# Kernel optimization log

Hardware: AMD Instinct MI355X
Metric: run time of the kernel (lower is better)

The kernel has to match this reference:

```python
import jax, jax.numpy as jnp
import numpy as np

N_HEAD = 8
N_FEAT = 256
CHUNK = 64          # window/chunk size N
D_K = N_FEAT // N_HEAD
SCALE = D_K ** (-0.5)
B_ = 2048           # batch * nChunkNum
NCHUNK = 128        # nChunkNum (B_ % NCHUNK == 0)


def setup_inputs() -> dict:
    key = jax.random.key(0)
    ks = jax.random.split(key, 12)
    f32 = jnp.float32
    query = jax.random.normal(ks[0], (B_, CHUNK, N_FEAT), f32)
    key_t = jax.random.normal(ks[1], (B_, CHUNK, N_FEAT), f32)
    value = jax.random.normal(ks[2], (B_, CHUNK, N_FEAT), f32)
    # padding mask (B_, time2): multiplicative 0/1 floats
    mask = jax.random.randint(ks[3], (B_, CHUNK), 0, 2).astype(f32)
    # shifted-chunk additive mask (nChunkNum, N, N): 0 for neighbors, -100 otherwise
    cm_bin = jax.random.randint(ks[4], (NCHUNK, CHUNK, CHUNK), 0, 2)
    chunk_mask = jnp.where(cm_bin == 1, 0.0, -100.0).astype(f32)
    def lin(k):
        return jax.random.normal(k, (N_FEAT, N_FEAT), f32) * 0.02
    Wq, Wk, Wv, Wo = lin(ks[5]), lin(ks[6]), lin(ks[7]), lin(ks[8])
    bq = jnp.zeros((N_FEAT,), f32)
    bk = jnp.zeros((N_FEAT,), f32)
    bv = jnp.zeros((N_FEAT,), f32)
    bo = jnp.zeros((N_FEAT,), f32)
    rpb_table = jax.random.normal(ks[9], (2 * CHUNK - 1, N_HEAD), f32) * 0.02
    return {"query": query, "key": key_t, "value": value, "mask": mask,
            "chunk_mask": chunk_mask, "Wq": Wq, "bq": bq, "Wk": Wk, "bk": bk,
            "Wv": Wv, "bv": bv, "Wo": Wo, "bo": bo, "rpb_table": rpb_table}


def _rel_pos_index():
    # index[i, j] = (i - j) + CHUNK - 1, shape (N, N)
    w = jnp.arange(CHUNK)
    return w[:, None] - w[None, :] + (CHUNK - 1)


def reference(query, key, value, mask, chunk_mask, Wq, bq, Wk, bk, Wv, bv, Wo, bo, rpb_table):
    B, N, _ = query.shape
    # qkv projections -> (B, h, N, d_k)
    def proj(x, W, b):
        y = x @ W.T + b
        return y.reshape(B, N, N_HEAD, D_K).transpose(0, 2, 1, 3)
    q = proj(query, Wq, bq)
    k = proj(key, Wk, bk)
    v = proj(value, Wv, bv)
    # windowed attention scores (B, h, N, N)
    scores = jnp.einsum("bhid,bhjd->bhij", q, k) * SCALE
    # relative position bias: gather (N, N, h) -> (h, N, N)
    rpb = rpb_table[_rel_pos_index()].transpose(2, 0, 1)
    scores = scores + rpb[None]
    # padding mask: multiply, then fill zeros with -100 (as in torch source)
    scores = scores * mask[:, None, None, :]
    scores = jnp.where(scores == 0, jnp.float32(-100.0), scores)
    # additive shifted-chunk mask
    nC = chunk_mask.shape[0]
    scores = scores.reshape(B // nC, nC, N_HEAD, N, N) + chunk_mask[None, :, None]
    scores = scores.reshape(B, N_HEAD, N, N)
    attn = jax.nn.softmax(scores, axis=-1)
    x = jnp.einsum("bhij,bhjd->bhid", attn, v)          # (B, h, N, d_k)
    x = x.transpose(0, 2, 1, 3).reshape(B, N, N_FEAT)     # (B, N, n_feat)
    return x @ Wo.T + bo
```

## Files before the change

### kernel.cpp

```cpp
#include <hip/hip_runtime.h>
#include <hip/hip_bf16.h>

typedef __bf16 bf16_t;
typedef __bf16 bf16x8 __attribute__((ext_vector_type(8)));
typedef __bf16 bf16x4 __attribute__((ext_vector_type(4)));
typedef float f32x4 __attribute__((ext_vector_type(4)));

#define OFF_A   0
#define OFF_B   32768
#define OFF_RPB 65536
#define OFF_CMM (65536 + 4096)
#define OFF_PAD (65536 + 4096 + 512)
#define SMEM_BYTES (65536 + 4096 + 512 + 8)

__device__ __forceinline__ int tile_off(int r, int c) {
  return (r << 9) + ((((c >> 3) ^ (r & 7)) << 4) | ((c & 7) << 1));
}
__device__ __forceinline__ int vt_off(int d, int j) {
  return (d << 7) + ((((j >> 3) ^ (d & 7)) << 4) | ((j & 7) << 1));
}
__device__ __forceinline__ int ps_off(int i, int j) {
  return (i << 6) + ((((j >> 3) ^ ((i >> 1) & 3)) << 4) | ((j & 7) << 1));
}

template <int UNROLL>
__device__ __forceinline__ void stage_x(const float* __restrict__ src, char* __restrict__ dst, int tid) {
  const float4* s4 = (const float4*)src;
#pragma unroll
  for (int kk = 0; kk < 8; kk += UNROLL) {
    float4 v[UNROLL];
#pragma unroll
    for (int u = 0; u < UNROLL; ++u) v[u] = s4[tid + ((kk + u) << 9)];
#pragma unroll
    for (int u = 0; u < UNROLL; ++u) {
      int f = tid + ((kk + u) << 9);
      int row = f >> 6;
      int col = (f & 63) << 2;
      bf16x4 p;
      p[0] = (bf16_t)v[u].x; p[1] = (bf16_t)v[u].y; p[2] = (bf16_t)v[u].z; p[3] = (bf16_t)v[u].w;
      *(bf16x4*)(dst + tile_off(row, col)) = p;
    }
  }
}

__device__ __forceinline__ void gemm_tile(const char* __restrict__ sA, const bf16_t* __restrict__ W,
                                          int cb, int l15, int g, f32x4 acc[4][2]) {
#pragma unroll
  for (int kt = 0; kt < 8; ++kt) {
    bf16x8 a[4];
#pragma unroll
    for (int mt = 0; mt < 4; ++mt)
      a[mt] = *(const bf16x8*)(sA + tile_off(mt*16 + l15, kt*32 + g*8));
#pragma unroll
    for (int nt = 0; nt < 2; ++nt) {
      bf16x8 bw = *(const bf16x8*)(W + (cb + nt*16 + l15)*256 + kt*32 + g*8);
#pragma unroll
      for (int mt = 0; mt < 4; ++mt)
        acc[mt][nt] = __builtin_amdgcn_mfma_f32_16x16x32_bf16(a[mt], bw, acc[mt][nt], 0, 0, 0);
    }
  }
}

__device__ __forceinline__ void gemm_tile2(const char* __restrict__ sA, const char* __restrict__ sB,
                                           const bf16_t* __restrict__ W0, const bf16_t* __restrict__ W1,
                                           int cb, int l15, int g,
                                           f32x4 acc0[4][2], f32x4 acc1[4][2]) {
  const bf16_t* w0p = W0 + (cb + l15)*256 + g*8;
  const bf16_t* w1p = W1 + (cb + l15)*256 + g*8;
#pragma unroll
  for (int kt = 0; kt < 8; ++kt) {
    bf16x8 a0[4], a1[4];
#pragma unroll
    for (int mt = 0; mt < 4; ++mt) {
      a0[mt] = *(const bf16x8*)(sA + tile_off(mt*16 + l15, kt*32 + g*8));
      a1[mt] = *(const bf16x8*)(sB + tile_off(mt*16 + l15, kt*32 + g*8));
    }
#pragma unroll
    for (int nt = 0; nt < 2; ++nt) {
      bf16x8 bw0 = *(const bf16x8*)(w0p + nt*16*256 + kt*32);
      bf16x8 bw1 = *(const bf16x8*)(w1p + nt*16*256 + kt*32);
#pragma unroll
      for (int mt = 0; mt < 4; ++mt) {
        acc0[mt][nt] = __builtin_amdgcn_mfma_f32_16x16x32_bf16(a0[mt], bw0, acc0[mt][nt], 0, 0, 0);
        acc1[mt][nt] = __builtin_amdgcn_mfma_f32_16x16x32_bf16(a1[mt], bw1, acc1[mt][nt], 0, 0, 0);
      }
    }
  }
}

__global__ __launch_bounds__(512, 2)
void chunk_attn_kernel(
    const float* __restrict__ qg, const float* __restrict__ kg, const float* __restrict__ vg,
    const float* __restrict__ maskg, const float* __restrict__ cmg,
    const float* __restrict__ bq, const float* __restrict__ bk, const float* __restrict__ bv,
    const float* __restrict__ bo, const float* __restrict__ rpbg,
    const bf16_t* __restrict__ Wb, float* __restrict__ outg) {
  extern __shared__ char sm[];
  char*  bufA  = sm + OFF_A;
  char*  bufB  = sm + OFF_B;
  float* sRpb  = (float*)(sm + OFF_RPB);
  char*  sCmm  = sm + OFF_CMM;

  const int b = blockIdx.x, tid = threadIdx.x;
  const int wave = tid >> 6, lane = tid & 63, l15 = lane & 15, g = lane >> 4;
  const int cb = wave << 5;
  char* scr = bufB + (wave << 12);

  for (int i = tid; i < 1016; i += 512) sRpb[((i & 7) << 7) + (i >> 3)] = rpbg[i];
  {
    if (wave == 0) {
      float mv = maskg[(b << 6) + lane];
      unsigned long long bm = __ballot(mv == 0.0f);
      if (lane == 0) *(unsigned long long*)(sm + OFF_PAD) = bm;
    }
    const float* cmb = cmg + ((size_t)(b & 127) << 12);
#pragma unroll
    for (int it = 0; it < 8; ++it) {
      int row = (wave << 3) + it;
      float cv = cmb[(row << 6) + lane];
      unsigned long long bm = __ballot(cv < -50.0f);
      if (lane == 0) *(unsigned long long*)(sCmm + (row << 3)) = bm;
    }
  }
  stage_x<4>(qg + (size_t)b*16384, bufA, tid);
  stage_x<4>(kg + (size_t)b*16384, bufB, tid);
  __syncthreads();

  {
    f32x4 qacc[4][2] = {}, kacc[4][2] = {};
    gemm_tile2(bufA, bufB, Wb + 0*65536, Wb + 1*65536, cb, l15, g, qacc, kacc);
    __syncthreads();
    float bq0 = bq[cb+l15], bq1 = bq[cb+16+l15];
    float bk0 = bk[cb+l15], bk1 = bk[cb+16+l15];
#pragma unroll
    for (int mt = 0; mt < 4; ++mt)
#pragma unroll
      for (int nt = 0; nt < 2; ++nt)
#pragma unroll
        for (int r = 0; r < 4; ++r) {
          int row = mt*16 + g*4 + r, col = cb + nt*16 + l15;
          *(bf16_t*)(bufA + tile_off(row, col)) = (bf16_t)(qacc[mt][nt][r] + (nt ? bq1 : bq0));
          *(bf16_t*)(bufB + tile_off(row, col)) = (bf16_t)(kacc[mt][nt][r] + (nt ? bk1 : bk0));
        }
  }
  __asm__ volatile("s_waitcnt lgkmcnt(0)" ::: "memory");

  f32x4 St[4][4];
  {
    bf16x8 ka[4], qb[4];
#pragma unroll
    for (int t = 0; t < 4; ++t) {
      ka[t] = *(const bf16x8*)(bufB + tile_off(t*16 + l15, cb + g*8));
      qb[t] = *(const bf16x8*)(bufA + tile_off(t*16 + l15, cb + g*8));
    }
    const f32x4 z = {};
#pragma unroll
    for (int mj = 0; mj < 4; ++mj)
#pragma unroll
      for (int ni = 0; ni < 4; ++ni)
        St[mj][ni] = __builtin_amdgcn_mfma_f32_16x16x32_bf16(ka[mj], qb[ni], z, 0, 0, 0);
  }

  const float* rpbw = sRpb + (wave << 7);
  unsigned long long padm = *(const unsigned long long*)(sm + OFF_PAD);
  unsigned int padl = (unsigned int)padm, padh = (unsigned int)(padm >> 32);
#pragma unroll
  for (int mj = 0; mj < 4; ++mj) {
    unsigned int pw = (mj >= 2) ? padh : padl;
#pragma unroll
    for (int ni = 0; ni < 4; ++ni) {
      int i = ni*16 + l15;
      unsigned long long cmm = *(const unsigned long long*)(sCmm + (i << 3));
      unsigned int cw = (mj >= 2) ? (unsigned int)(cmm >> 32) : (unsigned int)cmm;
#pragma unroll
      for (int r = 0; r < 4; ++r) {
        int j = mj*16 + g*4 + r;
        int sh = j & 31;
        float s1 = St[mj][ni][r] * 0.17677669529663689f + rpbw[i - j + 63];
        float base = ((pw >> sh) & 1u) ? -100.0f : s1;
        St[mj][ni][r] = ((cw >> sh) & 1u) ? base - 100.0f : base;
      }
    }
  }

  float rinv[4];
  bf16x4 pbf[4][4];
#pragma unroll
  for (int ni = 0; ni < 4; ++ni) {
    float m = -1e30f;
#pragma unroll
    for (int mj = 0; mj < 4; ++mj)
#pragma unroll
      for (int r = 0; r < 4; ++r) m = fmaxf(m, St[mj][ni][r]);
    m = fmaxf(m, __shfl_xor(m, 16));
    m = fmaxf(m, __shfl_xor(m, 32));
    float s = 0.0f;
#pragma unroll
    for (int mj = 0; mj < 4; ++mj)
#pragma unroll
      for (int r = 0; r < 4; ++r) {
        float p = __expf(St[mj][ni][r] - m);
        pbf[mj][ni][r] = (bf16_t)p;
        s += p;
      }
    s += __shfl_xor(s, 16);
    s += __shfl_xor(s, 32);
    rinv[ni] = 1.0f / s;
  }

  __syncthreads();
  stage_x<4>(vg + (size_t)b*16384, bufB, tid);
  __syncthreads();

  {
    f32x4 vacc[4][2] = {};
    gemm_tile(bufB, Wb + 2*65536, cb, l15, g, vacc);
    float b0 = bv[cb+l15], b1 = bv[cb+16+l15];
#pragma unroll
    for (int nt = 0; nt < 2; ++nt)
#pragma unroll
      for (int mt = 0; mt < 4; ++mt) {
        bf16x4 p;
#pragma unroll
        for (int r = 0; r < 4; ++r) p[r] = (bf16_t)(vacc[mt][nt][r] + (nt ? b1 : b0));
        *(bf16x4*)(bufA + vt_off(cb + nt*16 + l15, mt*16 + g*4)) = p;
      }
  }
  __syncthreads();

  f32x4 Xa[2][4] = {};
#pragma unroll
  for (int h2 = 0; h2 < 2; ++h2) {
#pragma unroll
    for (int mj = 2*h2; mj < 2*h2 + 2; ++mj)
#pragma unroll
      for (int ni = 0; ni < 4; ++ni)
        *(bf16x4*)(scr + ps_off(ni*16 + l15, (mj & 1)*16 + g*4)) = pbf[mj][ni];
    __asm__ volatile("s_waitcnt lgkmcnt(0)" ::: "memory");
    bf16x8 va[2], pb[4];
#pragma unroll
    for (int mtd = 0; mtd < 2; ++mtd)
      va[mtd] = *(const bf16x8*)(bufA + vt_off(cb + mtd*16 + l15, h2*32 + g*8));
#pragma unroll
    for (int ni = 0; ni < 4; ++ni)
      pb[ni] = *(const bf16x8*)(scr + ps_off(ni*16 + l15, g*8));
#pragma unroll
    for (int mtd = 0; mtd < 2; ++mtd)
#pragma unroll
      for (int ni = 0; ni < 4; ++ni)
        Xa[mtd][ni] = __builtin_amdgcn_mfma_f32_16x16x32_bf16(va[mtd], pb[ni], Xa[mtd][ni], 0, 0, 0);
  }

  __syncthreads();
#pragma unroll
  for (int mtd = 0; mtd < 2; ++mtd)
#pragma unroll
    for (int ni = 0; ni < 4; ++ni)
#pragma unroll
      for (int r = 0; r < 4; ++r) {
        int dloc = mtd*16 + g*4 + r;
        int i = ni*16 + l15;
        *(bf16_t*)(bufB + tile_off(i, cb + dloc)) = (bf16_t)(Xa[mtd][ni][r] * rinv[ni]);
      }
  __syncthreads();

  {
    f32x4 acc[4][2] = {};
    gemm_tile(bufB, Wb + 3*65536, cb, l15, g, acc);
    float b0 = bo[cb+l15], b1 = bo[cb+16+l15];
    float* ob = outg + (size_t)b * 16384;
#pragma unroll
    for (int mt = 0; mt < 4; ++mt)
#pragma unroll
      for (int nt = 0; nt < 2; ++nt)
#pragma unroll
        for (int r = 0; r < 4; ++r)
          ob[(mt*16 + g*4 + r)*256 + cb + nt*16 + l15] = acc[mt][nt][r] + (nt ? b1 : b0);
  }
}

__global__ void cvt_weights(const float* __restrict__ Wq, const float* __restrict__ Wk,
                            const float* __restrict__ Wv, const float* __restrict__ Wo,
                            bf16_t* __restrict__ dst) {
  int idx = blockIdx.x * 256 + threadIdx.x;
  int which = idx >> 14;
  int off = idx & 16383;
  const float* src = (which == 0) ? Wq : (which == 1) ? Wk : (which == 2) ? Wv : Wo;
  float4 v = ((const float4*)src)[off];
  bf16x4 p;
  p[0] = (bf16_t)v.x; p[1] = (bf16_t)v.y; p[2] = (bf16_t)v.z; p[3] = (bf16_t)v.w;
  *(bf16x4*)(dst + which*65536 + off*4) = p;
}

extern "C" void kernel_launch(void* const* d_in, const int* in_sizes, int n_in,
                              void* d_out, int out_size, void* d_ws, size_t ws_size,
                              hipStream_t stream) {
  (void)in_sizes; (void)n_in; (void)out_size; (void)ws_size;
  const float* qg  = (const float*)d_in[0];
  const float* kg  = (const float*)d_in[1];
  const float* vg  = (const float*)d_in[2];
  const float* mg  = (const float*)d_in[3];
  const float* cmg = (const float*)d_in[4];
  const float* Wq  = (const float*)d_in[5];
  const float* bq  = (const float*)d_in[6];
  const float* Wk  = (const float*)d_in[7];
  const float* bk  = (const float*)d_in[8];
  const float* Wv  = (const float*)d_in[9];
  const float* bv  = (const float*)d_in[10];
  const float* Wo  = (const float*)d_in[11];
  const float* bo  = (const float*)d_in[12];
  const float* rpb = (const float*)d_in[13];
  bf16_t* Wb = (bf16_t*)d_ws;
  float* outg = (float*)d_out;

  hipFuncSetAttribute(reinterpret_cast<const void*>(chunk_attn_kernel),
                      hipFuncAttributeMaxDynamicSharedMemorySize, SMEM_BYTES);
  cvt_weights<<<256, 256, 0, stream>>>(Wq, Wk, Wv, Wo, Wb);
  chunk_attn_kernel<<<2048, 512, SMEM_BYTES, stream>>>(qg, kg, vg, mg, cmg,
      bq, bk, bv, bo, rpb, Wb, outg);
}
```

Before: 251.8 us.

## Halve block size to 256 threads with each wave handling two heads

The kernel now launches 4 waves per block instead of 8. Each wave processes two heads (column blocks cb and cb+128) in every stage: QK projection, scores and softmax, V projection, PV product and output projection. The first head's Q/K results are held in registers until after the barrier. This means fewer threads share each block's barriers and each wave gets more MFMA work to hide latency, at the cost of much higher register pressure and possibly lower occupancy, since LDS use stays near 70KB per block.

```diff
diff --git a/kernel.cpp b/kernel.cpp
--- a/kernel.cpp
+++ b/kernel.cpp
@@ -27,13 +27,13 @@
 __device__ __forceinline__ void stage_x(const float* __restrict__ src, char* __restrict__ dst, int tid) {
   const float4* s4 = (const float4*)src;
 #pragma unroll
-  for (int kk = 0; kk < 8; kk += UNROLL) {
+  for (int kk = 0; kk < 16; kk += UNROLL) {
     float4 v[UNROLL];
 #pragma unroll
-    for (int u = 0; u < UNROLL; ++u) v[u] = s4[tid + ((kk + u) << 9)];
+    for (int u = 0; u < UNROLL; ++u) v[u] = s4[tid + ((kk + u) << 8)];
 #pragma unroll
     for (int u = 0; u < UNROLL; ++u) {
-      int f = tid + ((kk + u) << 9);
+      int f = tid + ((kk + u) << 8);
       int row = f >> 6;
       int col = (f & 63) << 2;
       bf16x4 p;
@@ -45,6 +45,7 @@
 
 __device__ __forceinline__ void gemm_tile(const char* __restrict__ sA, const bf16_t* __restrict__ W,
                                           int cb, int l15, int g, f32x4 acc[4][2]) {
+  const bf16_t* wp = W + (cb + l15)*256 + g*8;
 #pragma unroll
   for (int kt = 0; kt < 8; ++kt) {
     bf16x8 a[4];
@@ -53,7 +54,7 @@
       a[mt] = *(const bf16x8*)(sA + tile_off(mt*16 + l15, kt*32 + g*8));
 #pragma unroll
     for (int nt = 0; nt < 2; ++nt) {
-      bf16x8 bw = *(const bf16x8*)(W + (cb + nt*16 + l15)*256 + kt*32 + g*8);
+      bf16x8 bw = *(const bf16x8*)(wp + nt*16*256 + kt*32);
 #pragma unroll
       for (int mt = 0; mt < 4; ++mt)
         acc[mt][nt] = __builtin_amdgcn_mfma_f32_16x16x32_bf16(a[mt], bw, acc[mt][nt], 0, 0, 0);
@@ -72,8 +73,9 @@
     bf16x8 a0[4], a1[4];
 #pragma unroll
     for (int mt = 0; mt < 4; ++mt) {
-      a0[mt] = *(const bf16x8*)(sA + tile_off(mt*16 + l15, kt*32 + g*8));
-      a1[mt] = *(const bf16x8*)(sB + tile_off(mt*16 + l15, kt*32 + g*8));
+      int off = tile_off(mt*16 + l15, kt*32 + g*8);
+      a0[mt] = *(const bf16x8*)(sA + off);
+      a1[mt] = *(const bf16x8*)(sB + off);
     }
 #pragma unroll
     for (int nt = 0; nt < 2; ++nt) {
@@ -88,7 +90,7 @@
   }
 }
 
-__global__ __launch_bounds__(512, 2)
+__global__ __launch_bounds__(256, 2)
 void chunk_attn_kernel(
     const float* __restrict__ qg, const float* __restrict__ kg, const float* __restrict__ vg,
     const float* __restrict__ maskg, const float* __restrict__ cmg,
@@ -103,10 +105,8 @@
 
   const int b = blockIdx.x, tid = threadIdx.x;
   const int wave = tid >> 6, lane = tid & 63, l15 = lane & 15, g = lane >> 4;
-  const int cb = wave << 5;
-  char* scr = bufB + (wave << 12);
-
-  for (int i = tid; i < 1016; i += 512) sRpb[((i & 7) << 7) + (i >> 3)] = rpbg[i];
+
+  for (int i = tid; i < 1016; i += 256) sRpb[((i & 7) << 7) + (i >> 3)] = rpbg[i];
   {
     if (wave == 0) {
       float mv = maskg[(b << 6) + lane];
@@ -115,8 +115,8 @@
     }
     const float* cmb = cmg + ((size_t)(b & 127) << 12);
 #pragma unroll
-    for (int it = 0; it < 8; ++it) {
-      int row = (wave << 3) + it;
+    for (int it = 0; it < 16; ++it) {
+      int row = (wave << 4) + it;
       float cv = cmb[(row << 6) + lane];
       unsigned long long bm = __ballot(cv < -50.0f);
       if (lane == 0) *(unsigned long long*)(sCmm + (row << 3)) = bm;
@@ -126,7 +126,25 @@
   stage_x<4>(kg + (size_t)b*16384, bufB, tid);
   __syncthreads();
 
+  bf16x4 q0bf[4][2], k0bf[4][2];
   {
+    int cb = wave << 5;
+    f32x4 qacc[4][2] = {}, kacc[4][2] = {};
+    gemm_tile2(bufA, bufB, Wb + 0*65536, Wb + 1*65536, cb, l15, g, qacc, kacc);
+    float bq0 = bq[cb+l15], bq1 = bq[cb+16+l15];
+    float bk0 = bk[cb+l15], bk1 = bk[cb+16+l15];
+#pragma unroll
+    for (int mt = 0; mt < 4; ++mt)
+#pragma unroll
+      for (int nt = 0; nt < 2; ++nt)
+#pragma unroll
+        for (int r = 0; r < 4; ++r) {
+          q0bf[mt][nt][r] = (bf16_t)(qacc[mt][nt][r] + (nt ? bq1 : bq0));
+          k0bf[mt][nt][r] = (bf16_t)(kacc[mt][nt][r] + (nt ? bk1 : bk0));
+        }
+  }
+  {
+    int cb = (wave + 4) << 5;
     f32x4 qacc[4][2] = {}, kacc[4][2] = {};
     gemm_tile2(bufA, bufB, Wb + 0*65536, Wb + 1*65536, cb, l15, g, qacc, kacc);
     __syncthreads();
@@ -138,81 +156,87 @@
       for (int nt = 0; nt < 2; ++nt)
 #pragma unroll
         for (int r = 0; r < 4; ++r) {
-          int row = mt*16 + g*4 + r, col = cb + nt*16 + l15;
-          *(bf16_t*)(bufA + tile_off(row, col)) = (bf16_t)(qacc[mt][nt][r] + (nt ? bq1 : bq0));
-          *(bf16_t*)(bufB + tile_off(row, col)) = (bf16_t)(kacc[mt][nt][r] + (nt ? bk1 : bk0));
+          int row = mt*16 + g*4 + r, col = nt*16 + l15;
+          *(bf16_t*)(bufA + tile_off(row, cb + col)) = (bf16_t)(qacc[mt][nt][r] + (nt ? bq1 : bq0));
+          *(bf16_t*)(bufB + tile_off(row, cb + col)) = (bf16_t)(kacc[mt][nt][r] + (nt ? bk1 : bk0));
+          *(bf16_t*)(bufA + tile_off(row, (wave << 5) + col)) = q0bf[mt][nt][r];
+          *(bf16_t*)(bufB + tile_off(row, (wave << 5) + col)) = k0bf[mt][nt][r];
         }
   }
   __asm__ volatile("s_waitcnt lgkmcnt(0)" ::: "memory");
 
-  f32x4 St[4][4];
-  {
-    bf16x8 ka[4], qb[4];
-#pragma unroll
-    for (int t = 0; t < 4; ++t) {
-      ka[t] = *(const bf16x8*)(bufB + tile_off(t*16 + l15, cb + g*8));
-      qb[t] = *(const bf16x8*)(bufA + tile_off(t*16 + l15, cb + g*8));
-    }
-    const f32x4 z = {};
-#pragma unroll
-    for (int mj = 0; mj < 4; ++mj)
-#pragma unroll
-      for (int ni = 0; ni < 4; ++ni)
-        St[mj][ni] = __builtin_amdgcn_mfma_f32_16x16x32_bf16(ka[mj], qb[ni], z, 0, 0, 0);
-  }
-
-  const float* rpbw = sRpb + (wave << 7);
   unsigned long long padm = *(const unsigned long long*)(sm + OFF_PAD);
   unsigned int padl = (unsigned int)padm, padh = (unsigned int)(padm >> 32);
-#pragma unroll
-  for (int mj = 0; mj < 4; ++mj) {
-    unsigned int pw = (mj >= 2) ? padh : padl;
+  float rinv[2][4];
+  bf16x4 pbf[2][4][4];
+#pragma unroll
+  for (int hh = 0; hh < 2; ++hh) {
+    int cb = (wave + 4*hh) << 5;
+    const float* rpbw = sRpb + ((wave + 4*hh) << 7);
+    f32x4 St[4][4];
+    {
+      bf16x8 ka[4], qb[4];
+#pragma unroll
+      for (int t = 0; t < 4; ++t) {
+        ka[t] = *(const bf16x8*)(bufB + tile_off(t*16 + l15, cb + g*8));
+        qb[t] = *(const bf16x8*)(bufA + tile_off(t*16 + l15, cb + g*8));
+      }
+      const f32x4 z = {};
+#pragma unroll
+      for (int mj = 0; mj < 4; ++mj)
+#pragma unroll
+        for (int ni = 0; ni < 4; ++ni)
+          St[mj][ni] = __builtin_amdgcn_mfma_f32_16x16x32_bf16(ka[mj], qb[ni], z, 0, 0, 0);
+    }
+#pragma unroll
+    for (int mj = 0; mj < 4; ++mj) {
+      unsigned int pw = (mj >= 2) ? padh : padl;
+#pragma unroll
+      for (int ni = 0; ni < 4; ++ni) {
+        int i = ni*16 + l15;
+        unsigned long long cmm = *(const unsigned long long*)(sCmm + (i << 3));
+        unsigned int cw = (mj >= 2) ? (unsigned int)(cmm >> 32) : (unsigned int)cmm;
+#pragma unroll
+        for (int r = 0; r < 4; ++r) {
+          int j = mj*16 + g*4 + r;
+          int sh = j & 31;
+          float s1 = St[mj][ni][r] * 0.17677669529663689f + rpbw[i - j + 63];
+          float base = ((pw >> sh) & 1u) ? -100.0f : s1;
+          St[mj][ni][r] = ((cw >> sh) & 1u) ? base - 100.0f : base;
+        }
+      }
+    }
 #pragma unroll
     for (int ni = 0; ni < 4; ++ni) {
-      int i = ni*16 + l15;
-      unsigned long long cmm = *(const unsigned long long*)(sCmm + (i << 3));
-      unsigned int cw = (mj >= 2) ? (unsigned int)(cmm >> 32) : (unsigned int)cmm;
-#pragma unroll
-      for (int r = 0; r < 4; ++r) {
-        int j = mj*16 + g*4 + r;
-        int sh = j & 31;
-        float s1 = St[mj][ni][r] * 0.17677669529663689f + rpbw[i - j + 63];
-        float base = ((pw >> sh) & 1u) ? -100.0f : s1;
-        St[mj][ni][r] = ((cw >> sh) & 1u) ? base - 100.0f : base;
-      }
-    }
-  }
-
-  float rinv[4];
-  bf16x4 pbf[4][4];
-#pragma unroll
-  for (int ni = 0; ni < 4; ++ni) {
-    float m = -1e30f;
-#pragma unroll
-    for (int mj = 0; mj < 4; ++mj)
-#pragma unroll
-      for (int r = 0; r < 4; ++r) m = fmaxf(m, St[mj][ni][r]);
-    m = fmaxf(m, __shfl_xor(m, 16));
-    m = fmaxf(m, __shfl_xor(m, 32));
-    float s = 0.0f;
-#pragma unroll
-    for (int mj = 0; mj < 4; ++mj)
-#pragma unroll
-      for (int r = 0; r < 4; ++r) {
-        float p = __expf(St[mj][ni][r] - m);
-        pbf[mj][ni][r] = (bf16_t)p;
-        s += p;
-      }
-    s += __shfl_xor(s, 16);
-    s += __shfl_xor(s, 32);
-    rinv[ni] = 1.0f / s;
+      float m = -1e30f;
+#pragma unroll
+      for (int mj = 0; mj < 4; ++mj)
+#pragma unroll
+        for (int r = 0; r < 4; ++r) m = fmaxf(m, St[mj][ni][r]);
+      m = fmaxf(m, __shfl_xor(m, 16));
+      m = fmaxf(m, __shfl_xor(m, 32));
+      float s = 0.0f;
+#pragma unroll
+      for (int mj = 0; mj < 4; ++mj)
+#pragma unroll
+        for (int r = 0; r < 4; ++r) {
+          float p = __expf(St[mj][ni][r] - m);
+          pbf[hh][mj][ni][r] = (bf16_t)p;
+          s += p;
+        }
+      s += __shfl_xor(s, 16);
+      s += __shfl_xor(s, 32);
+      rinv[hh][ni] = 1.0f / s;
+    }
   }
 
   __syncthreads();
   stage_x<4>(vg + (size_t)b*16384, bufB, tid);
   __syncthreads();
 
-  {
+#pragma unroll
+  for (int hh = 0; hh < 2; ++hh) {
+    int cb = (wave + 4*hh) << 5;
     f32x4 vacc[4][2] = {};
     gemm_tile(bufB, Wb + 2*65536, cb, l15, g, vacc);
     float b0 = bv[cb+l15], b1 = bv[cb+16+l15];
@@ -228,47 +252,62 @@
   }
   __syncthreads();
 
-  f32x4 Xa[2][4] = {};
-#pragma unroll
-  for (int h2 = 0; h2 < 2; ++h2) {
-#pragma unroll
-    for (int mj = 2*h2; mj < 2*h2 + 2; ++mj)
+  f32x4 Xa[2][2][4];
+#pragma unroll
+  for (int hh = 0; hh < 2; ++hh) {
+    int cb = (wave + 4*hh) << 5;
+    char* scr = bufB + (((wave << 1) | hh) << 12);
+#pragma unroll
+    for (int mtd = 0; mtd < 2; ++mtd)
+#pragma unroll
+      for (int ni = 0; ni < 4; ++ni) Xa[hh][mtd][ni] = (f32x4){};
+#pragma unroll
+    for (int h2 = 0; h2 < 2; ++h2) {
+#pragma unroll
+      for (int mj = 2*h2; mj < 2*h2 + 2; ++mj)
+#pragma unroll
+        for (int ni = 0; ni < 4; ++ni)
+          *(bf16x4*)(scr + ps_off(ni*16 + l15, (mj & 1)*16 + g*4)) = pbf[hh][mj][ni];
+      __asm__ volatile("s_waitcnt lgkmcnt(0)" ::: "memory");
+      bf16x8 va[2], pb[4];
+#pragma unroll
+      for (int mtd = 0; mtd < 2; ++mtd)
+        va[mtd] = *(const bf16x8*)(bufA + vt_off(cb + mtd*16 + l15, h2*32 + g*8));
 #pragma unroll
       for (int ni = 0; ni < 4; ++ni)
-        *(bf16x4*)(scr + ps_off(ni*16 + l15, (mj & 1)*16 + g*4)) = pbf[mj][ni];
-    __asm__ volatile("s_waitcnt lgkmcnt(0)" ::: "memory");
-    bf16x8 va[2], pb[4];
+        pb[ni] = *(const bf16x8*)(scr + ps_off(ni*16 + l15, g*8));
+#pragma unroll
+      for (int mtd = 0; mtd < 2; ++mtd)
+#pragma unroll
+        for (int ni = 0; ni < 4; ++ni)
+          Xa[hh][mtd][ni] = __builtin_amdgcn_mfma_f32_16x16x32_bf16(va[mtd], pb[ni], Xa[hh][mtd][ni], 0, 0, 0);
+    }
+  }
+
+  __syncthreads();
+#pragma unroll
+  for (int hh = 0; hh < 2; ++hh) {
+    int cb = (wave + 4*hh) << 5;
 #pragma unroll
     for (int mtd = 0; mtd < 2; ++mtd)
-      va[mtd] = *(const bf16x8*)(bufA + vt_off(cb + mtd*16 + l15, h2*32 + g*8));
-#pragma unroll
-    for (int ni = 0; ni < 4; ++ni)
-      pb[ni] = *(const bf16x8*)(scr + ps_off(ni*16 + l15, g*8));
-#pragma unroll
-    for (int mtd = 0; mtd < 2; ++mtd)
 #pragma unroll
       for (int ni = 0; ni < 4; ++ni)
-        Xa[mtd][ni] = __builtin_amdgcn_mfma_f32_16x16x32_bf16(va[mtd], pb[ni], Xa[mtd][ni], 0, 0, 0);
-  }
-
-  __syncthreads();
-#pragma unroll
-  for (int mtd = 0; mtd < 2; ++mtd)
-#pragma unroll
-    for (int ni = 0; ni < 4; ++ni)
-#pragma unroll
-      for (int r = 0; r < 4; ++r) {
-        int dloc = mtd*16 + g*4 + r;
-        int i = ni*16 + l15;
-        *(bf16_t*)(bufB + tile_off(i, cb + dloc)) = (bf16_t)(Xa[mtd][ni][r] * rinv[ni]);
-      }
-  __syncthreads();
-
-  {
+#pragma unroll
+        for (int r = 0; r < 4; ++r) {
+          int dloc = mtd*16 + g*4 + r;
+          int i = ni*16 + l15;
+          *(bf16_t*)(bufB + tile_off(i, cb + dloc)) = (bf16_t)(Xa[hh][mtd][ni][r] * rinv[hh][ni]);
+        }
+  }
+  __syncthreads();
+
+  float* ob = outg + (size_t)b * 16384;
+#pragma unroll
+  for (int hh = 0; hh < 2; ++hh) {
+    int cb = (wave + 4*hh) << 5;
     f32x4 acc[4][2] = {};
     gemm_tile(bufB, Wb + 3*65536, cb, l15, g, acc);
     float b0 = bo[cb+l15], b1 = bo[cb+16+l15];
-    float* ob = outg + (size_t)b * 16384;
 #pragma unroll
     for (int mt = 0; mt < 4; ++mt)
 #pragma unroll
@@ -316,6 +355,6 @@
   hipFuncSetAttribute(reinterpret_cast<const void*>(chunk_attn_kernel),
                       hipFuncAttributeMaxDynamicSharedMemorySize, SMEM_BYTES);
   cvt_weights<<<256, 256, 0, stream>>>(Wq, Wk, Wv, Wo, Wb);
-  chunk_attn_kernel<<<2048, 512, SMEM_BYTES, stream>>>(qg, kg, vg, mg, cmg,
+  chunk_attn_kernel<<<2048, 256, SMEM_BYTES, stream>>>(qg, kg, vg, mg, cmg,
       bq, bk, bv, bo, rpb, Wb, outg);
 }
```

After: 342.5 us. 36.0% more time.
